# Optimization experiments

Hardware: AMD Instinct MI355X
Metric: run time of the kernel (lower is better)

Reference implementation:

```python
import jax, jax.numpy as jnp
import numpy as np

WS = 8       # window size
NH = 6       # num heads
SHIFT = 4    # ws//2 since index=1 (shifted)
EPS = 1e-6


def _rel_pos_index(ws):
    coords = np.stack(np.meshgrid(np.arange(ws), np.arange(ws), indexing='ij'))  # (2,ws,ws)
    cf = coords.reshape(2, -1)
    rel = (cf[:, :, None] - cf[:, None, :]).transpose(1, 2, 0)  # (N,N,2)
    rel[..., 0] += ws - 1
    rel[..., 1] += ws - 1
    rel[..., 0] *= 2 * ws - 1
    return rel.sum(-1)  # (N,N) int


def _attn_mask(H, W, ws, shift):
    img = np.zeros((H, W))
    slices = (slice(0, -ws), slice(-ws, -shift), slice(-shift, None))
    cnt = 0
    for h in slices:
        for w in slices:
            img[h, w] = cnt
            cnt += 1
    mw = img.reshape(H // ws, ws, W // ws, ws).transpose(0, 2, 1, 3).reshape(-1, ws * ws)
    am = mw[:, None, :] - mw[:, :, None]  # (nW,N,N): unsqueeze(1) - unsqueeze(2)
    return np.where(am != 0, -100.0, 0.0).astype(np.float32)


def layernorm2d(x, w, b):
    mu = x.mean(1, keepdims=True)
    var = ((x - mu) ** 2).mean(1, keepdims=True)
    y = (x - mu) / jnp.sqrt(var + EPS)
    return w[None, :, None, None] * y + b[None, :, None, None]


def window_partition(x, ws):
    B, C, H, W = x.shape
    x = x.reshape(B, C, H // ws, ws, W // ws, ws)
    return x.transpose(0, 2, 4, 3, 5, 1).reshape(-1, ws * ws, C)


def window_reverse(win, ws, H, W):
    B = win.shape[0] // ((H // ws) * (W // ws))
    x = win.reshape(B, H // ws, W // ws, ws, ws, -1)
    return x.transpose(0, 5, 1, 3, 2, 4).reshape(B, -1, H, W)


def shifted_window_attn(x, qkv_w, qkv_b, proj_w, proj_b, rpb_table):
    B, C, H, W = x.shape
    N = WS * WS
    hd = C // NH
    scale = hd ** -0.5
    # faithful to original: raw reshape BCHW->BHWC (reinterpretation), roll, reshape back
    x = jnp.roll(x.reshape(B, H, W, C), (-SHIFT, -SHIFT), (1, 2)).reshape(B, C, H, W)
    win = window_partition(x, WS)  # (B_, N, C)
    B_ = win.shape[0]
    qkv = (win @ qkv_w + qkv_b).reshape(B_, N, 3, NH, hd).transpose(2, 0, 3, 1, 4)
    q, k, v = qkv[0] * scale, qkv[1], qkv[2]
    attn = jnp.einsum('bhnd,bhmd->bhnm', q, k)  # (B_,NH,N,N)
    rpi = _rel_pos_index(WS)
    bias = rpb_table[rpi.reshape(-1)].reshape(N, N, NH).transpose(2, 0, 1)
    attn = attn + bias[None]
    mask = jnp.asarray(_attn_mask(H, W, WS, SHIFT))  # (nW,N,N)
    nW = mask.shape[0]
    attn = attn.reshape(B_ // nW, nW, NH, N, N) + mask[None, :, None]
    attn = jax.nn.softmax(attn.reshape(B_, NH, N, N), axis=-1)
    out = jnp.einsum('bhnm,bhmd->bhnd', attn, v).transpose(0, 2, 1, 3).reshape(B_, N, C)
    out = out @ proj_w + proj_b
    return window_reverse(out, WS, H, W)


def channel_attention(y, ca_w, ca_b):
    gap = y.mean((2, 3))  # (B,C)
    s = jnp.einsum('bc,oc->bo', gap, ca_w) + ca_b  # 1x1 conv on pooled feature
    return s[:, :, None, None]


def mlp(y, fc1_w, fc1_b, fc2_w, fc2_b):
    B, C, H, W = y.shape
    t = y.transpose(0, 2, 3, 1)  # (B,H,W,C)
    t = jax.nn.gelu(t @ fc1_w + fc1_b, approximate=False)
    t = t @ fc2_w + fc2_b
    return t.transpose(0, 3, 1, 2)


def setup_inputs() -> dict:
    key = jax.random.key(0)
    ks = jax.random.split(key, 8)
    C, H, W, B = 192, 256, 256, 2
    hid = 2 * C
    sc = 0.02
    return {
        'x': jax.random.normal(ks[0], (B, C, H, W), jnp.float32),
        'norm1_w': jnp.ones((C,), jnp.float32),
        'norm1_b': jnp.zeros((C,), jnp.float32),
        'qkv_w': jax.random.normal(ks[1], (C, 3 * C), jnp.float32) * sc,
        'qkv_b': jnp.zeros((3 * C,), jnp.float32),
        'proj_w': jax.random.normal(ks[2], (C, C), jnp.float32) * sc,
        'proj_b': jnp.zeros((C,), jnp.float32),
        'rpb_table': jax.random.normal(ks[3], ((2 * WS - 1) ** 2, NH), jnp.float32) * sc,
        'ca_w': jax.random.normal(ks[4], (C, C), jnp.float32) * sc,
        'ca_b': jnp.zeros((C,), jnp.float32),
        'norm2_w': jnp.ones((C,), jnp.float32),
        'norm2_b': jnp.zeros((C,), jnp.float32),
        'fc1_w': jax.random.normal(ks[5], (C, hid), jnp.float32) * sc,
        'fc1_b': jnp.zeros((hid,), jnp.float32),
        'fc2_w': jax.random.normal(ks[6], (hid, C), jnp.float32) * sc,
        'fc2_b': jnp.zeros((C,), jnp.float32),
    }


def reference(x, norm1_w, norm1_b, qkv_w, qkv_b, proj_w, proj_b, rpb_table,
              ca_w, ca_b, norm2_w, norm2_b, fc1_w, fc1_b, fc2_w, fc2_b):
    y = layernorm2d(x, norm1_w, norm1_b)
    y = shifted_window_attn(y, qkv_w, qkv_b, proj_w, proj_b, rpb_table)
    y = y * channel_attention(y, ca_w, ca_b)
    x = x + y
    y2 = mlp(layernorm2d(x, norm2_w, norm2_b), fc1_w, fc1_b, fc2_w, fc2_b)
    return x + y2
```

## Files before the change

kernel.cpp:

```cpp
#include <hip/hip_runtime.h>
#include <hip/hip_bf16.h>
#include <stdint.h>

#define C_   192
#define H_   256
#define W_   256
#define HW_  65536
#define CHW  12582912
#define NH_  6
#define HID_ 384

typedef __attribute__((ext_vector_type(8))) __bf16 bf16x8;
typedef __attribute__((ext_vector_type(4))) float  fx4;

__device__ __forceinline__ uint16_t f2bf(float f) {
  uint32_t u = __builtin_bit_cast(uint32_t, f);
  u += 0x7fffu + ((u >> 16) & 1u);
  return (uint16_t)(u >> 16);
}
__device__ __forceinline__ float bf2f(uint16_t h) {
  uint32_t u = ((uint32_t)h) << 16;
  return __builtin_bit_cast(float, u);
}
__device__ __forceinline__ uint32_t pk2(float a, float b) {
  return (uint32_t)f2bf(a) | ((uint32_t)f2bf(b) << 16);
}
__device__ __forceinline__ bf16x8 ld8(const uint16_t* p) {
  uint4 v = *reinterpret_cast<const uint4*>(p);
  return __builtin_bit_cast(bf16x8, v);
}
__device__ __forceinline__ fx4 mfma16(bf16x8 a, bf16x8 b, fx4 c) {
  return __builtin_amdgcn_mfma_f32_16x16x32_bf16(a, b, c, 0, 0, 0);
}

__global__ __launch_bounds__(256) void prep_kernel(
    const float* __restrict__ qkv_w, const float* __restrict__ proj_w,
    const float* __restrict__ fc1_w, const float* __restrict__ fc2_w,
    const float* __restrict__ rpb,
    uint16_t* __restrict__ qkv_wt, uint16_t* __restrict__ proj_wt,
    uint16_t* __restrict__ fc1_wt, uint16_t* __restrict__ fc2_wt,
    float* __restrict__ rpbb) {
  int tid = blockIdx.x * 256 + threadIdx.x;
  if (tid < 576 * 192) {
    int f = tid / 192, k = tid % 192;
    qkv_wt[tid] = f2bf(qkv_w[k * 576 + f]);
  }
  int t1 = tid - 576 * 192;
  if (t1 >= 0 && t1 < 192 * 192) {
    int f = t1 / 192, k = t1 % 192;
    proj_wt[t1] = f2bf(proj_w[k * 192 + f]);
  }
  int t2 = t1 - 192 * 192;
  if (t2 >= 0 && t2 < 384 * 192) {
    int f = t2 / 192, k = t2 % 192;
    fc1_wt[t2] = f2bf(fc1_w[k * 384 + f]);
  }
  int t3 = t2 - 384 * 192;
  if (t3 >= 0 && t3 < 192 * 384) {
    int f = t3 / 384, k = t3 % 384;
    fc2_wt[t3] = f2bf(fc2_w[k * 192 + f]);
  }
  int t4 = t3 - 192 * 384;
  if (t4 >= 0 && t4 < 6 * 64 * 64) {
    int h = t4 / 4096, nm = t4 % 4096, n = nm / 64, m = nm % 64;
    int yn = n >> 3, xn = n & 7, ym = m >> 3, xm = m & 7;
    int idx = (yn - ym + 7) * 15 + (xn - xm + 7);
    rpbb[t4] = rpb[idx * NH_ + h];
  }
}

__global__ __launch_bounds__(256) void ln1_stats(const float* __restrict__ x,
                                                 float* __restrict__ mu,
                                                 float* __restrict__ rsig) {
  int t = blockIdx.x * 256 + threadIdx.x;
  int b = t >> 16, hw = t & 65535;
  const float* xp = x + (size_t)b * CHW + hw;
  float s = 0.f, sq = 0.f;
#pragma unroll 8
  for (int c = 0; c < C_; c++) {
    float v = xp[(size_t)c * HW_];
    s += v; sq += v * v;
  }
  float m = s * (1.0f / C_);
  float var = sq * (1.0f / C_) - m * m;
  mu[t] = m;
  rsig[t] = rsqrtf(var + 1e-6f);
}

__global__ __launch_bounds__(256) void ln1_apply_kernel(
    const float* __restrict__ x, const float* __restrict__ mu, const float* __restrict__ rsig,
    const float* __restrict__ n1w, const float* __restrict__ n1b,
    uint16_t* __restrict__ y_tok) {
  __shared__ __attribute__((aligned(16))) uint16_t tile[192 * 66];
  int wg = blockIdx.x;
  int b = wg >> 10, hw0 = (wg & 1023) << 6;
  int t = threadIdx.x;
  const float* xb = x + (size_t)b * CHW;
  const float* mub = mu + b * HW_;
  const float* rsb = rsig + b * HW_;
#pragma unroll 4
  for (int it = 0; it < 48; it++) {
    int id = it * 256 + t;
    int ca = id >> 6, pp = id & 63;
    int g = ca * 65536 + hw0 + pp;
    int h2 = g / 49152;
    int r = g - h2 * 49152;
    int w2 = r / 192;
    int c2 = r - w2 * 192;
    int f = ((h2 + 4) & 255) * 49152 + ((w2 + 4) & 255) * 192 + c2;
    int cnat = f >> 16;
    int hwn = f & 65535;
    float v = (xb[f] - mub[hwn]) * rsb[hwn] * n1w[cnat] + n1b[cnat];
    tile[ca * 66 + pp] = f2bf(v);
  }
  __syncthreads();
  uint16_t* yb = y_tok + ((size_t)(b * HW_ + hw0)) * C_;
#pragma unroll 4
  for (int it = 0; it < 48; it++) {
    int id = it * 256 + t;
    int pp = id / 192, ca = id - pp * 192;
    yb[id] = tile[ca * 66 + pp];
  }
}

__global__ __launch_bounds__(256, 2) void attn_kernel(
    const uint16_t* __restrict__ y_tok, const uint16_t* __restrict__ qkv_wt,
    const float* __restrict__ qkv_b, const uint16_t* __restrict__ proj_wt,
    const float* __restrict__ proj_b, const float* __restrict__ rpbb,
    uint16_t* __restrict__ y_attn, float* __restrict__ part) {
  __shared__ __attribute__((aligned(16))) uint16_t Qs[64 * 200];
  __shared__ __attribute__((aligned(16))) uint16_t Ks[64 * 200];
  __shared__ __attribute__((aligned(16))) uint16_t VT[32 * 72];
  __shared__ __attribute__((aligned(16))) uint16_t Ps[64 * 72];
  const int wg = blockIdx.x;
  const int b = wg >> 10, wid = wg & 1023;
  const int wh = wid >> 5, ww = wid & 31;
  const int t = threadIdx.x;
  const int w = t >> 6, l = t & 63;
  const int lane16 = l & 15, quad = l >> 4;
  const int trow = w * 16 + quad * 4;

  bf16x8 afr[4][6];
#pragma unroll
  for (int m = 0; m < 4; m++) {
    const int tok = m * 16 + lane16;
    const uint16_t* ap = y_tok +
        ((size_t)(b * HW_ + (wh * 8 + (tok >> 3)) * W_ + ww * 8 + (tok & 7))) * C_ + quad * 8;
#pragma unroll
    for (int k = 0; k < 6; k++) afr[m][k] = ld8(ap + k * 32);
  }

  const float scale = 0.17677669529663687f;
  uint32_t vpack[3][4][2];

#pragma unroll
  for (int j = 0; j < 3; j++) {
    const int nt = w + 4 * j;
    const uint16_t* bp = qkv_wt + (nt * 16 + lane16) * C_ + quad * 8;
    bf16x8 bfr[6];
#pragma unroll
    for (int k = 0; k < 6; k++) bfr[k] = ld8(bp + k * 32);
    fx4 acc[4];
#pragma unroll
    for (int m = 0; m < 4; m++) acc[m] = fx4{0.f, 0.f, 0.f, 0.f};
#pragma unroll
    for (int k = 0; k < 6; k++)
#pragma unroll
      for (int m = 0; m < 4; m++) acc[m] = mfma16(afr[m][k], bfr[k], acc[m]);
    const int f = nt * 16 + lane16;
    const float bias = qkv_b[f];
#pragma unroll
    for (int m = 0; m < 4; m++)
#pragma unroll
      for (int r = 0; r < 4; r++)
        Qs[(m * 16 + quad * 4 + r) * 200 + f] = f2bf((acc[m][r] + bias) * scale);
  }
#pragma unroll
  for (int j = 3; j < 6; j++) {
    const int nt = w + 4 * j;
    const uint16_t* bp = qkv_wt + (nt * 16 + lane16) * C_ + quad * 8;
    bf16x8 bfr[6];
#pragma unroll
    for (int k = 0; k < 6; k++) bfr[k] = ld8(bp + k * 32);
    fx4 acc[4];
#pragma unroll
    for (int m = 0; m < 4; m++) acc[m] = fx4{0.f, 0.f, 0.f, 0.f};
#pragma unroll
    for (int k = 0; k < 6; k++)
#pragma unroll
      for (int m = 0; m < 4; m++) acc[m] = mfma16(afr[m][k], bfr[k], acc[m]);
    const int f = nt * 16 + lane16;
    const float bias = qkv_b[f];
#pragma unroll
    for (int m = 0; m < 4; m++)
#pragma unroll
      for (int r = 0; r < 4; r++)
        Ks[(m * 16 + quad * 4 + r) * 200 + (f - 192)] = f2bf(acc[m][r] + bias);
  }
#pragma unroll
  for (int j = 6; j < 9; j++) {
    const int nt = w + 4 * j;
    const uint16_t* bp = qkv_wt + (nt * 16 + lane16) * C_ + quad * 8;
    bf16x8 bfr[6];
#pragma unroll
    for (int k = 0; k < 6; k++) bfr[k] = ld8(bp + k * 32);
    fx4 acc[4];
#pragma unroll
    for (int m = 0; m < 4; m++) acc[m] = fx4{0.f, 0.f, 0.f, 0.f};
#pragma unroll
    for (int k = 0; k < 6; k++)
#pragma unroll
      for (int m = 0; m < 4; m++) acc[m] = mfma16(afr[m][k], bfr[k], acc[m]);
    const float bias = qkv_b[nt * 16 + lane16];
    const int jv = j - 6;
#pragma unroll
    for (int m = 0; m < 4; m++) {
      vpack[jv][m][0] = pk2(acc[m][0] + bias, acc[m][1] + bias);
      vpack[jv][m][1] = pk2(acc[m][2] + bias, acc[m][3] + bias);
    }
  }

  const bool whe = (wh == 31), wwe = (ww == 31);

  for (int h = 0; h < 6; h++) {
    __syncthreads();
    {
      const int vt0 = 2 * h, vt1 = 2 * h + 1;
      if (w == (vt0 & 3)) {
        const int jv = vt0 >> 2;
#pragma unroll
        for (int m = 0; m < 4; m++) {
          uint2 vv; vv.x = vpack[jv][m][0]; vv.y = vpack[jv][m][1];
          *reinterpret_cast<uint2*>(&VT[lane16 * 72 + m * 16 + quad * 4]) = vv;
        }
      }
      if (w == (vt1 & 3)) {
        const int jv = vt1 >> 2;
#pragma unroll
        for (int m = 0; m < 4; m++) {
          uint2 vv; vv.x = vpack[jv][m][0]; vv.y = vpack[jv][m][1];
          *reinterpret_cast<uint2*>(&VT[(16 + lane16) * 72 + m * 16 + quad * 4]) = vv;
        }
      }
    }
    __syncthreads();

    const bf16x8 qa = ld8(&Qs[(w * 16 + lane16) * 200 + h * 32 + quad * 8]);
    fx4 sacc[4];
#pragma unroll
    for (int nt = 0; nt < 4; nt++) {
      const bf16x8 kb = ld8(&Ks[(nt * 16 + lane16) * 200 + h * 32 + quad * 8]);
      fx4 z = {0.f, 0.f, 0.f, 0.f};
      sacc[nt] = mfma16(qa, kb, z);
    }
    const float* rb = rpbb + h * 4096;
#pragma unroll
    for (int nt = 0; nt < 4; nt++) {
      const int ct = nt * 16 + lane16;
      const bool rbc = whe && ((ct >> 3) >= 4);
      const bool cbc = wwe && ((ct & 7) >= 4);
#pragma unroll
      for (int r = 0; r < 4; r++) {
        const int rt = trow + r;
        const bool rbr = whe && ((rt >> 3) >= 4);
        const bool cbr = wwe && ((rt & 7) >= 4);
        float v = sacc[nt][r] + rb[rt * 64 + ct];
        if (rbr != rbc || cbr != cbc) v -= 100.f;
        sacc[nt][r] = v;
      }
    }
    float sm[4];
#pragma unroll
    for (int r = 0; r < 4; r++) {
      float m = fmaxf(fmaxf(sacc[0][r], sacc[1][r]), fmaxf(sacc[2][r], sacc[3][r]));
      m = fmaxf(m, __shfl_xor(m, 1));
      m = fmaxf(m, __shfl_xor(m, 2));
      m = fmaxf(m, __shfl_xor(m, 4));
      m = fmaxf(m, __shfl_xor(m, 8));
      float s0 = 0.f;
#pragma unroll
      for (int nt = 0; nt < 4; nt++) {
        float e = exp2f((sacc[nt][r] - m) * 1.4426950408889634f);
        sacc[nt][r] = e; s0 += e;
      }
      s0 += __shfl_xor(s0, 1);
      s0 += __shfl_xor(s0, 2);
      s0 += __shfl_xor(s0, 4);
      s0 += __shfl_xor(s0, 8);
      sm[r] = s0;
    }
#pragma unroll
    for (int nt = 0; nt < 4; nt++)
#pragma unroll
      for (int r = 0; r < 4; r++)
        Ps[(trow + r) * 72 + nt * 16 + lane16] = f2bf(sacc[nt][r]);
    fx4 o0 = {0.f, 0.f, 0.f, 0.f}, o1 = {0.f, 0.f, 0.f, 0.f};
#pragma unroll
    for (int ks2 = 0; ks2 < 2; ks2++) {
      const bf16x8 pa = ld8(&Ps[(w * 16 + lane16) * 72 + ks2 * 32 + quad * 8]);
      const bf16x8 v0 = ld8(&VT[(lane16) * 72 + ks2 * 32 + quad * 8]);
      const bf16x8 v1 = ld8(&VT[(16 + lane16) * 72 + ks2 * 32 + quad * 8]);
      o0 = mfma16(pa, v0, o0);
      o1 = mfma16(pa, v1, o1);
    }
#pragma unroll
    for (int r = 0; r < 4; r++) {
      const float inv = 1.0f / sm[r];
      Qs[(trow + r) * 200 + h * 32 + lane16] = f2bf(o0[r] * inv);
      Qs[(trow + r) * 200 + h * 32 + 16 + lane16] = f2bf(o1[r] * inv);
    }
  }
  __syncthreads();

  bf16x8 ofr[4][6];
#pragma unroll
  for (int m = 0; m < 4; m++)
#pragma unroll
    for (int k = 0; k < 6; k++)
      ofr[m][k] = ld8(&Qs[(m * 16 + lane16) * 200 + k * 32 + quad * 8]);

  uint16_t* yb = y_attn + (size_t)b * HW_ * C_;
  uint32_t obase[4][4];
#pragma unroll
  for (int m = 0; m < 4; m++)
#pragma unroll
    for (int r = 0; r < 4; r++) {
      const int tok = m * 16 + quad * 4 + r;
      obase[m][r] = (uint32_t)(((wh * 8 + (tok >> 3)) * W_ + ww * 8 + (tok & 7)) * C_);
    }
#pragma unroll
  for (int j = 0; j < 3; j++) {
    const int nt = w + 4 * j;
    const uint16_t* bp = proj_wt + (nt * 16 + lane16) * C_ + quad * 8;
    bf16x8 bfr[6];
#pragma unroll
    for (int k = 0; k < 6; k++) bfr[k] = ld8(bp + k * 32);
    fx4 acc[4];
#pragma unroll
    for (int m = 0; m < 4; m++) acc[m] = fx4{0.f, 0.f, 0.f, 0.f};
#pragma unroll
    for (int k = 0; k < 6; k++)
#pragma unroll
      for (int m = 0; m < 4; m++) acc[m] = mfma16(ofr[m][k], bfr[k], acc[m]);
    const float pb = proj_b[nt * 16 + lane16];
    float cs = 0.f;
#pragma unroll
    for (int m = 0; m < 4; m++)
#pragma unroll
      for (int r = 0; r < 4; r++) {
        const float v = acc[m][r] + pb;
        yb[obase[m][r] + nt * 16 + lane16] = f2bf(v);
        cs += v;
      }
    cs += __shfl_xor(cs, 16);
    cs += __shfl_xor(cs, 32);
    if (l < 16) part[(size_t)wg * 192 + nt * 16 + lane16] = cs;
  }
}

__global__ __launch_bounds__(768) void ca_s_kernel(const float* __restrict__ part,
                                                   const float* __restrict__ ca_w,
                                                   const float* __restrict__ ca_b,
                                                   float* __restrict__ sbuf) {
  int b = blockIdx.x;
  int t = threadIdx.x;
  __shared__ float red[768];
  __shared__ float gap[192];
  int g = t / 192, c = t - g * 192;
  float s = 0.f;
#pragma unroll 8
  for (int i = g; i < 1024; i += 4) s += part[((size_t)b * 1024 + i) * 192 + c];
  red[t] = s;
  __syncthreads();
  if (t < 192)
    gap[t] = (red[t] + red[t + 192] + red[t + 384] + red[t + 576]) * (1.0f / 65536.0f);
  __syncthreads();
  if (t < 192) {
    float acc = ca_b[t];
#pragma unroll 8
    for (int c2 = 0; c2 < 192; c2++) acc += gap[c2] * ca_w[t * 192 + c2];
    sbuf[b * 192 + t] = acc;
  }
}

__global__ __launch_bounds__(256, 3) void resid_ln2(
    const float* __restrict__ x, const uint16_t* __restrict__ y_attn,
    const float* __restrict__ sbuf, const float* __restrict__ n2w,
    const float* __restrict__ n2b, uint16_t* __restrict__ t2) {
  __shared__ __attribute__((aligned(16))) float tile[192 * 66];
  __shared__ float red[512];
  __shared__ float mus[128];
  int wg = blockIdx.x;
  int b = wg >> 10, hw0 = (wg & 1023) << 6;
  int t = threadIdx.x;
#pragma unroll 4
  for (int it = 0; it < 48; it++) {
    int id = it * 256 + t;
    int c = id >> 6, p = id & 63;
    tile[c * 66 + p] = x[(size_t)b * CHW + (size_t)c * HW_ + hw0 + p];
  }
  __syncthreads();
#pragma unroll 4
  for (int it = 0; it < 48; it++) {
    int id = it * 256 + t;
    int p = id / 192, c = id - p * 192;
    float y = bf2f(y_attn[((size_t)(b * HW_ + hw0 + p)) * C_ + c]);
    tile[c * 66 + p] += sbuf[b * 192 + c] * y;
  }
  __syncthreads();
  {
    int p = t & 63, g = t >> 6;
    float s = 0.f, sq = 0.f;
    for (int c = g * 48; c < g * 48 + 48; c++) {
      float v = tile[c * 66 + p];
      s += v; sq += v * v;
    }
    red[g * 64 + p] = s;
    red[256 + g * 64 + p] = sq;
  }
  __syncthreads();
  if (t < 64) {
    float ss = red[t] + red[64 + t] + red[128 + t] + red[192 + t];
    float qq = red[256 + t] + red[320 + t] + red[384 + t] + red[448 + t];
    float m = ss * (1.0f / C_);
    float var = qq * (1.0f / C_) - m * m;
    mus[t] = m;
    mus[64 + t] = rsqrtf(var + 1e-6f);
  }
  __syncthreads();
#pragma unroll 4
  for (int it = 0; it < 48; it++) {
    int id = it * 256 + t;
    int p = id / 192, c = id - p * 192;
    float v = (tile[c * 66 + p] - mus[p]) * mus[64 + p] * n2w[c] + n2b[c];
    t2[((size_t)(b * HW_ + hw0 + p)) * C_ + c] = f2bf(v);
  }
}

__global__ __launch_bounds__(256, 3) void mlp_kernel(
    const uint16_t* __restrict__ t2, const uint16_t* __restrict__ fc1_wt,
    const float* __restrict__ fc1_b, const uint16_t* __restrict__ fc2_wt,
    const float* __restrict__ fc2_b, const float* __restrict__ x,
    const uint16_t* __restrict__ y_attn, const float* __restrict__ sbuf,
    float* __restrict__ out) {
  __shared__ __attribute__((aligned(16))) char smem[192 * 66 * 4];
  __shared__ float sarr[192];
  uint16_t* hbuf = (uint16_t*)smem;
  float* ftile = (float*)smem;
  int wg = blockIdx.x;
  int b = wg >> 10, hw0 = (wg & 1023) << 6;
  int t = threadIdx.x;
  int w = t >> 6, l = t & 63;
  int lane16 = l & 15, quad = l >> 4;
  if (t < 192) sarr[t] = sbuf[b * 192 + t];

  bf16x8 afr[4][6];
  const uint16_t* ab = t2 + ((size_t)(b * HW_ + hw0)) * C_;
#pragma unroll
  for (int m = 0; m < 4; m++) {
    const uint16_t* ap = ab + (m * 16 + lane16) * C_ + quad * 8;
#pragma unroll
    for (int k = 0; k < 6; k++) afr[m][k] = ld8(ap + k * 32);
  }

#pragma unroll
  for (int j = 0; j < 6; j++) {
    const int nt = w + 4 * j;
    const uint16_t* bp = fc1_wt + (nt * 16 + lane16) * C_ + quad * 8;
    bf16x8 bfr[6];
#pragma unroll
    for (int k = 0; k < 6; k++) bfr[k] = ld8(bp + k * 32);
    fx4 acc[4];
#pragma unroll
    for (int m = 0; m < 4; m++) acc[m] = fx4{0.f, 0.f, 0.f, 0.f};
#pragma unroll
    for (int k = 0; k < 6; k++)
#pragma unroll
      for (int m = 0; m < 4; m++) acc[m] = mfma16(afr[m][k], bfr[k], acc[m]);
    const float bias = fc1_b[nt * 16 + lane16];
#pragma unroll
    for (int m = 0; m < 4; m++)
#pragma unroll
      for (int r = 0; r < 4; r++) {
        float v = acc[m][r] + bias;
        float ge = 0.5f * v * (1.0f + erff(v * 0.7071067811865476f));
        hbuf[(m * 16 + quad * 4 + r) * 392 + nt * 16 + lane16] = f2bf(ge);
      }
  }
  __syncthreads();

  fx4 acc2[3][4];
#pragma unroll
  for (int j = 0; j < 3; j++)
#pragma unroll
    for (int m = 0; m < 4; m++) acc2[j][m] = fx4{0.f, 0.f, 0.f, 0.f};
#pragma unroll
  for (int kc = 0; kc < 4; kc++) {
    bf16x8 ha[4][3];
#pragma unroll
    for (int m = 0; m < 4; m++)
#pragma unroll
      for (int kk = 0; kk < 3; kk++)
        ha[m][kk] = ld8(&hbuf[(m * 16 + lane16) * 392 + kc * 96 + kk * 32 + quad * 8]);
#pragma unroll
    for (int j = 0; j < 3; j++) {
      const int nt = w + 4 * j;
      const uint16_t* bp = fc2_wt + (nt * 16 + lane16) * HID_ + kc * 96 + quad * 8;
#pragma unroll
      for (int kk = 0; kk < 3; kk++) {
        const bf16x8 bb = ld8(bp + kk * 32);
#pragma unroll
        for (int m = 0; m < 4; m++) acc2[j][m] = mfma16(ha[m][kk], bb, acc2[j][m]);
      }
    }
  }
  __syncthreads();

#pragma unroll
  for (int j = 0; j < 3; j++) {
    const int nt = w + 4 * j;
    const float bias = fc2_b[nt * 16 + lane16];
#pragma unroll
    for (int m = 0; m < 4; m++) {
      float* fp = &ftile[(nt * 16 + lane16) * 66 + m * 16 + quad * 4];
      float2 a = {acc2[j][m][0] + bias, acc2[j][m][1] + bias};
      float2 b2 = {acc2[j][m][2] + bias, acc2[j][m][3] + bias};
      *reinterpret_cast<float2*>(fp) = a;
      *reinterpret_cast<float2*>(fp + 2) = b2;
    }
  }
  __syncthreads();
#pragma unroll 4
  for (int it = 0; it < 48; it++) {
    int id = it * 256 + t;
    int p = id / 192, c = id - p * 192;
    float y = bf2f(y_attn[((size_t)(b * HW_ + hw0 + p)) * C_ + c]);
    ftile[c * 66 + p] += sarr[c] * y;
  }
  __syncthreads();
#pragma unroll 4
  for (int it = 0; it < 48; it++) {
    int id = it * 256 + t;
    int c = id >> 6, p = id & 63;
    size_t gi = (size_t)b * CHW + (size_t)c * HW_ + hw0 + p;
    out[gi] = x[gi] + ftile[c * 66 + p];
  }
}

extern "C" void kernel_launch(void* const* d_in, const int* in_sizes, int n_in,
                              void* d_out, int out_size, void* d_ws, size_t ws_size,
                              hipStream_t stream) {
  const float* x      = (const float*)d_in[0];
  const float* n1w    = (const float*)d_in[1];
  const float* n1b    = (const float*)d_in[2];
  const float* qkv_w  = (const float*)d_in[3];
  const float* qkv_b  = (const float*)d_in[4];
  const float* proj_w = (const float*)d_in[5];
  const float* proj_b = (const float*)d_in[6];
  const float* rpb    = (const float*)d_in[7];
  const float* ca_w   = (const float*)d_in[8];
  const float* ca_b   = (const float*)d_in[9];
  const float* n2w    = (const float*)d_in[10];
  const float* n2b    = (const float*)d_in[11];
  const float* fc1_w  = (const float*)d_in[12];
  const float* fc1_b  = (const float*)d_in[13];
  const float* fc2_w  = (const float*)d_in[14];
  const float* fc2_b  = (const float*)d_in[15];
  float* out = (float*)d_out;

  char* ws = (char*)d_ws;
  uint16_t* y_tok   = (uint16_t*)(ws + 0);
  uint16_t* y_attn  = (uint16_t*)(ws + 50331648);
  uint16_t* t2      = y_tok;
  float*    mu      = (float*)   (ws + 100663296);
  float*    rsig    = (float*)   (ws + 101187584);
  uint16_t* qkv_wt  = (uint16_t*)(ws + 101711872);
  uint16_t* proj_wt = (uint16_t*)(ws + 101933056);
  uint16_t* fc1_wt  = (uint16_t*)(ws + 102006784);
  uint16_t* fc2_wt  = (uint16_t*)(ws + 102154240);
  float*    rpbb    = (float*)   (ws + 102301696);
  float*    part    = (float*)   (ws + 102400000);
  float*    sbuf    = (float*)   (ws + 103972864);

  hipLaunchKernelGGL(prep_kernel, dim3(1248), dim3(256), 0, stream,
                     qkv_w, proj_w, fc1_w, fc2_w, rpb, qkv_wt, proj_wt, fc1_wt, fc2_wt, rpbb);
  hipLaunchKernelGGL(ln1_stats, dim3(512), dim3(256), 0, stream, x, mu, rsig);
  hipLaunchKernelGGL(ln1_apply_kernel, dim3(2048), dim3(256), 0, stream,
                     x, mu, rsig, n1w, n1b, y_tok);
  hipLaunchKernelGGL(attn_kernel, dim3(2048), dim3(256), 0, stream,
                     y_tok, qkv_wt, qkv_b, proj_wt, proj_b, rpbb, y_attn, part);
  hipLaunchKernelGGL(ca_s_kernel, dim3(2), dim3(768), 0, stream, part, ca_w, ca_b, sbuf);
  hipLaunchKernelGGL(resid_ln2, dim3(2048), dim3(256), 0, stream,
                     x, y_attn, sbuf, n2w, n2b, t2);
  hipLaunchKernelGGL(mlp_kernel, dim3(2048), dim3(256), 0, stream,
                     t2, fc1_wt, fc1_b, fc2_wt, fc2_b, x, y_attn, sbuf, out);
}
```

Baseline: 577.5 us.

## Fuse residual+LayerNorm2 into MLP kernel and fold norm affine into fc1

Merges resid_ln2 and mlp_kernel into one 512-thread kernel. LayerNorm is applied in registers straight from the shared tile into MFMA A-fragments, so the bf16 t2 intermediate is never written to or read back from global memory. The norm2 weight and bias are folded into fc1 weights and a precomputed bias in prep, and erf-GELU is replaced by a tanh approximation built on exp2/rcp. Global loads are vectorized. The cost is changed numerics from the tanh GELU and the folded bf16 weights, plus higher register and LDS pressure at 512 threads.

```diff
diff --git a/kernel.cpp b/kernel.cpp
--- a/kernel.cpp
+++ b/kernel.cpp
@@ -11,6 +11,7 @@
 #define HID_ 384
 
 typedef __attribute__((ext_vector_type(8))) __bf16 bf16x8;
+typedef __attribute__((ext_vector_type(8))) uint16_t u16x8;
 typedef __attribute__((ext_vector_type(4))) float  fx4;
 
 __device__ __forceinline__ uint16_t f2bf(float f) {
@@ -32,14 +33,23 @@
 __device__ __forceinline__ fx4 mfma16(bf16x8 a, bf16x8 b, fx4 c) {
   return __builtin_amdgcn_mfma_f32_16x16x32_bf16(a, b, c, 0, 0, 0);
 }
+__device__ __forceinline__ float gelu_f(float v) {
+  float c2 = v * v;
+  float u = __builtin_fmaf(c2, 0.044715f, 1.0f) * v;
+  float e = exp2f(u * 2.3022084f);
+  float th = 1.0f - 2.0f * __builtin_amdgcn_rcpf(1.0f + e);
+  float hv = 0.5f * v;
+  return __builtin_fmaf(hv, th, hv);
+}
 
 __global__ __launch_bounds__(256) void prep_kernel(
     const float* __restrict__ qkv_w, const float* __restrict__ proj_w,
     const float* __restrict__ fc1_w, const float* __restrict__ fc2_w,
-    const float* __restrict__ rpb,
+    const float* __restrict__ rpb, const float* __restrict__ n2w,
+    const float* __restrict__ n2b, const float* __restrict__ fc1_b,
     uint16_t* __restrict__ qkv_wt, uint16_t* __restrict__ proj_wt,
     uint16_t* __restrict__ fc1_wt, uint16_t* __restrict__ fc2_wt,
-    float* __restrict__ rpbb) {
+    float* __restrict__ rpbb, float* __restrict__ b1f) {
   int tid = blockIdx.x * 256 + threadIdx.x;
   if (tid < 576 * 192) {
     int f = tid / 192, k = tid % 192;
@@ -53,7 +63,7 @@
   int t2 = t1 - 192 * 192;
   if (t2 >= 0 && t2 < 384 * 192) {
     int f = t2 / 192, k = t2 % 192;
-    fc1_wt[t2] = f2bf(fc1_w[k * 384 + f]);
+    fc1_wt[t2] = f2bf(fc1_w[k * 384 + f] * n2w[k]);
   }
   int t3 = t2 - 384 * 192;
   if (t3 >= 0 && t3 < 192 * 384) {
@@ -66,6 +76,12 @@
     int yn = n >> 3, xn = n & 7, ym = m >> 3, xm = m & 7;
     int idx = (yn - ym + 7) * 15 + (xn - xm + 7);
     rpbb[t4] = rpb[idx * NH_ + h];
+  }
+  int t5 = t4 - 6 * 64 * 64;
+  if (t5 >= 0 && t5 < 384) {
+    float acc = fc1_b[t5];
+    for (int c = 0; c < 192; c++) acc = __builtin_fmaf(n2b[c], fc1_w[c * 384 + t5], acc);
+    b1f[t5] = acc;
   }
 }
 
@@ -383,36 +399,59 @@
   }
 }
 
-__global__ __launch_bounds__(256, 3) void resid_ln2(
+__global__ __launch_bounds__(512, 6) void fused_mlp(
     const float* __restrict__ x, const uint16_t* __restrict__ y_attn,
-    const float* __restrict__ sbuf, const float* __restrict__ n2w,
-    const float* __restrict__ n2b, uint16_t* __restrict__ t2) {
-  __shared__ __attribute__((aligned(16))) float tile[192 * 66];
+    const float* __restrict__ sbuf,
+    const uint16_t* __restrict__ fc1_wt, const float* __restrict__ b1f,
+    const uint16_t* __restrict__ fc2_wt, const float* __restrict__ fc2_b,
+    float* __restrict__ out) {
+  __shared__ __attribute__((aligned(16))) char smem[192 * 66 * 4];
   __shared__ float red[512];
   __shared__ float mus[128];
-  int wg = blockIdx.x;
-  int b = wg >> 10, hw0 = (wg & 1023) << 6;
-  int t = threadIdx.x;
-#pragma unroll 4
-  for (int it = 0; it < 48; it++) {
-    int id = it * 256 + t;
-    int c = id >> 6, p = id & 63;
-    tile[c * 66 + p] = x[(size_t)b * CHW + (size_t)c * HW_ + hw0 + p];
-  }
-  __syncthreads();
-#pragma unroll 4
-  for (int it = 0; it < 48; it++) {
-    int id = it * 256 + t;
-    int p = id / 192, c = id - p * 192;
-    float y = bf2f(y_attn[((size_t)(b * HW_ + hw0 + p)) * C_ + c]);
-    tile[c * 66 + p] += sbuf[b * 192 + c] * y;
-  }
-  __syncthreads();
+  __shared__ float sarr[192];
+  float* tileXR = (float*)smem;
+  uint16_t* hbuf = (uint16_t*)smem;
+  float* ftile = (float*)smem;
+  const int wg = blockIdx.x;
+  const int b = wg >> 10, hw0 = (wg & 1023) << 6;
+  const int t = threadIdx.x;
+  const int w = t >> 6, l = t & 63;
+  const int lane16 = l & 15, quad = l >> 4;
+
+  if (t < 192) sarr[t] = sbuf[b * 192 + t];
+
+  const float* xb = x + (size_t)b * CHW + hw0;
+#pragma unroll
+  for (int i = 0; i < 12; i++) {
+    int id = i * 512 + t;
+    int c = id >> 5, p2 = id & 31;
+    float2 v = *reinterpret_cast<const float2*>(xb + (size_t)c * HW_ + p2 * 2);
+    *reinterpret_cast<float2*>(&tileXR[c * 66 + p2 * 2]) = v;
+  }
+  __syncthreads();
+
   {
+    const int p = t & 63, qb = (t >> 6) * 3;
+    const uint16_t* yr = y_attn + ((size_t)(b * HW_ + hw0 + p)) * C_;
+#pragma unroll
+    for (int i = 0; i < 3; i++) {
+      int q = qb + i;
+      u16x8 uv = __builtin_bit_cast(u16x8, ld8(yr + q * 8));
+#pragma unroll
+      for (int j = 0; j < 8; j++) {
+        int c = q * 8 + j;
+        tileXR[c * 66 + p] += sarr[c] * bf2f(uv[j]);
+      }
+    }
+  }
+  __syncthreads();
+
+  if (t < 256) {
     int p = t & 63, g = t >> 6;
     float s = 0.f, sq = 0.f;
+#pragma unroll 8
     for (int c = g * 48; c < g * 48 + 48; c++) {
-      float v = tile[c * 66 + p];
+      float v = tileXR[c * 66 + p];
       s += v; sq += v * v;
     }
     red[g * 64 + p] = s;
@@ -428,89 +467,81 @@
     mus[64 + t] = rsqrtf(var + 1e-6f);
   }
   __syncthreads();
+
+  bf16x8 afr[6];
+  const int m1 = w & 3;
+  {
+    const int p = m1 * 16 + lane16;
+    const float mu = mus[p], rs = mus[64 + p];
+#pragma unroll
+    for (int k = 0; k < 6; k++) {
+      uint32_t u0, u1, u2, u3;
+      {
+        int c = k * 32 + quad * 8;
+        float a0 = (tileXR[(c + 0) * 66 + p] - mu) * rs;
+        float a1 = (tileXR[(c + 1) * 66 + p] - mu) * rs;
+        float a2 = (tileXR[(c + 2) * 66 + p] - mu) * rs;
+        float a3 = (tileXR[(c + 3) * 66 + p] - mu) * rs;
+        float a4 = (tileXR[(c + 4) * 66 + p] - mu) * rs;
+        float a5 = (tileXR[(c + 5) * 66 + p] - mu) * rs;
+        float a6 = (tileXR[(c + 6) * 66 + p] - mu) * rs;
+        float a7 = (tileXR[(c + 7) * 66 + p] - mu) * rs;
+        u0 = pk2(a0, a1); u1 = pk2(a2, a3); u2 = pk2(a4, a5); u3 = pk2(a6, a7);
+      }
+      uint4 uv = {u0, u1, u2, u3};
+      afr[k] = __builtin_bit_cast(bf16x8, uv);
+    }
+  }
+  __syncthreads();
+
+  {
+    const int ntb = (w >> 2) * 12;
 #pragma unroll 4
-  for (int it = 0; it < 48; it++) {
-    int id = it * 256 + t;
-    int p = id / 192, c = id - p * 192;
-    float v = (tile[c * 66 + p] - mus[p]) * mus[64 + p] * n2w[c] + n2b[c];
-    t2[((size_t)(b * HW_ + hw0 + p)) * C_ + c] = f2bf(v);
-  }
-}
-
-__global__ __launch_bounds__(256, 3) void mlp_kernel(
-    const uint16_t* __restrict__ t2, const uint16_t* __restrict__ fc1_wt,
-    const float* __restrict__ fc1_b, const uint16_t* __restrict__ fc2_wt,
-    const float* __restrict__ fc2_b, const float* __restrict__ x,
-    const uint16_t* __restrict__ y_attn, const float* __restrict__ sbuf,
-    float* __restrict__ out) {
-  __shared__ __attribute__((aligned(16))) char smem[192 * 66 * 4];
-  __shared__ float sarr[192];
-  uint16_t* hbuf = (uint16_t*)smem;
-  float* ftile = (float*)smem;
-  int wg = blockIdx.x;
-  int b = wg >> 10, hw0 = (wg & 1023) << 6;
-  int t = threadIdx.x;
-  int w = t >> 6, l = t & 63;
-  int lane16 = l & 15, quad = l >> 4;
-  if (t < 192) sarr[t] = sbuf[b * 192 + t];
-
-  bf16x8 afr[4][6];
-  const uint16_t* ab = t2 + ((size_t)(b * HW_ + hw0)) * C_;
-#pragma unroll
-  for (int m = 0; m < 4; m++) {
-    const uint16_t* ap = ab + (m * 16 + lane16) * C_ + quad * 8;
-#pragma unroll
-    for (int k = 0; k < 6; k++) afr[m][k] = ld8(ap + k * 32);
-  }
-
-#pragma unroll
-  for (int j = 0; j < 6; j++) {
-    const int nt = w + 4 * j;
-    const uint16_t* bp = fc1_wt + (nt * 16 + lane16) * C_ + quad * 8;
-    bf16x8 bfr[6];
-#pragma unroll
-    for (int k = 0; k < 6; k++) bfr[k] = ld8(bp + k * 32);
-    fx4 acc[4];
-#pragma unroll
-    for (int m = 0; m < 4; m++) acc[m] = fx4{0.f, 0.f, 0.f, 0.f};
-#pragma unroll
-    for (int k = 0; k < 6; k++)
-#pragma unroll
-      for (int m = 0; m < 4; m++) acc[m] = mfma16(afr[m][k], bfr[k], acc[m]);
-    const float bias = fc1_b[nt * 16 + lane16];
-#pragma unroll
-    for (int m = 0; m < 4; m++)
-#pragma unroll
-      for (int r = 0; r < 4; r++) {
-        float v = acc[m][r] + bias;
-        float ge = 0.5f * v * (1.0f + erff(v * 0.7071067811865476f));
-        hbuf[(m * 16 + quad * 4 + r) * 392 + nt * 16 + lane16] = f2bf(ge);
-      }
-  }
-  __syncthreads();
-
-  fx4 acc2[3][4];
+    for (int j = 0; j < 12; j++) {
+      const int nt = ntb + j;
+      const uint16_t* bp = fc1_wt + (nt * 16 + lane16) * C_ + quad * 8;
+      bf16x8 bfr[6];
+#pragma unroll
+      for (int k = 0; k < 6; k++) bfr[k] = ld8(bp + k * 32);
+      fx4 acc = {0.f, 0.f, 0.f, 0.f};
+#pragma unroll
+      for (int k = 0; k < 6; k++) acc = mfma16(bfr[k], afr[k], acc);
+      const fx4 b4 = *reinterpret_cast<const fx4*>(b1f + nt * 16 + quad * 4);
+      float g0 = gelu_f(acc[0] + b4[0]);
+      float g1 = gelu_f(acc[1] + b4[1]);
+      float g2 = gelu_f(acc[2] + b4[2]);
+      float g3 = gelu_f(acc[3] + b4[3]);
+      uint2 wv = {pk2(g0, g1), pk2(g2, g3)};
+      *reinterpret_cast<uint2*>(&hbuf[(m1 * 16 + lane16) * 392 + nt * 16 + quad * 4]) = wv;
+    }
+  }
+  __syncthreads();
+
+  const int mh2 = w >> 2;
+  const int ntr2 = w & 3;
+  fx4 acc2[3][2];
 #pragma unroll
   for (int j = 0; j < 3; j++)
 #pragma unroll
-    for (int m = 0; m < 4; m++) acc2[j][m] = fx4{0.f, 0.f, 0.f, 0.f};
+    for (int mi = 0; mi < 2; mi++) acc2[j][mi] = fx4{0.f, 0.f, 0.f, 0.f};
 #pragma unroll
   for (int kc = 0; kc < 4; kc++) {
-    bf16x8 ha[4][3];
-#pragma unroll
-    for (int m = 0; m < 4; m++)
+    bf16x8 ha[2][3];
+#pragma unroll
+    for (int mi = 0; mi < 2; mi++)
 #pragma unroll
       for (int kk = 0; kk < 3; kk++)
-        ha[m][kk] = ld8(&hbuf[(m * 16 + lane16) * 392 + kc * 96 + kk * 32 + quad * 8]);
+        ha[mi][kk] = ld8(&hbuf[((mh2 * 2 + mi) * 16 + lane16) * 392 + kc * 96 + kk * 32 + quad * 8]);
 #pragma unroll
     for (int j = 0; j < 3; j++) {
-      const int nt = w + 4 * j;
-      const uint16_t* bp = fc2_wt + (nt * 16 + lane16) * HID_ + kc * 96 + quad * 8;
+      const int nt2 = ntr2 * 3 + j;
+      const uint16_t* bp = fc2_wt + (nt2 * 16 + lane16) * HID_ + kc * 96 + quad * 8;
 #pragma unroll
       for (int kk = 0; kk < 3; kk++) {
         const bf16x8 bb = ld8(bp + kk * 32);
 #pragma unroll
-        for (int m = 0; m < 4; m++) acc2[j][m] = mfma16(ha[m][kk], bb, acc2[j][m]);
+        for (int mi = 0; mi < 2; mi++)
+          acc2[j][mi] = mfma16(ha[mi][kk], bb, acc2[j][mi]);
       }
     }
   }
@@ -518,32 +549,44 @@
 
 #pragma unroll
   for (int j = 0; j < 3; j++) {
-    const int nt = w + 4 * j;
-    const float bias = fc2_b[nt * 16 + lane16];
-#pragma unroll
-    for (int m = 0; m < 4; m++) {
-      float* fp = &ftile[(nt * 16 + lane16) * 66 + m * 16 + quad * 4];
-      float2 a = {acc2[j][m][0] + bias, acc2[j][m][1] + bias};
-      float2 b2 = {acc2[j][m][2] + bias, acc2[j][m][3] + bias};
-      *reinterpret_cast<float2*>(fp) = a;
-      *reinterpret_cast<float2*>(fp + 2) = b2;
-    }
-  }
-  __syncthreads();
-#pragma unroll 4
-  for (int it = 0; it < 48; it++) {
-    int id = it * 256 + t;
-    int p = id / 192, c = id - p * 192;
-    float y = bf2f(y_attn[((size_t)(b * HW_ + hw0 + p)) * C_ + c]);
-    ftile[c * 66 + p] += sarr[c] * y;
-  }
-  __syncthreads();
-#pragma unroll 4
-  for (int it = 0; it < 48; it++) {
-    int id = it * 256 + t;
-    int c = id >> 6, p = id & 63;
-    size_t gi = (size_t)b * CHW + (size_t)c * HW_ + hw0 + p;
-    out[gi] = x[gi] + ftile[c * 66 + p];
+    const int nt2 = ntr2 * 3 + j;
+    const float bias = fc2_b[nt2 * 16 + lane16];
+#pragma unroll
+    for (int mi = 0; mi < 2; mi++) {
+      float* fp = &ftile[(nt2 * 16 + lane16) * 66 + (mh2 * 2 + mi) * 16 + quad * 4];
+      float2 aa = {acc2[j][mi][0] + bias, acc2[j][mi][1] + bias};
+      float2 bb2 = {acc2[j][mi][2] + bias, acc2[j][mi][3] + bias};
+      *reinterpret_cast<float2*>(fp) = aa;
+      *reinterpret_cast<float2*>(fp + 2) = bb2;
+    }
+  }
+  __syncthreads();
+
+  {
+    const int p = t & 63, qb = (t >> 6) * 3;
+    const uint16_t* yr = y_attn + ((size_t)(b * HW_ + hw0 + p)) * C_;
+#pragma unroll
+    for (int i = 0; i < 3; i++) {
+      int q = qb + i;
+      u16x8 uv = __builtin_bit_cast(u16x8, ld8(yr + q * 8));
+#pragma unroll
+      for (int j = 0; j < 8; j++) {
+        int c = q * 8 + j;
+        ftile[c * 66 + p] += sarr[c] * bf2f(uv[j]);
+      }
+    }
+  }
+  __syncthreads();
+
+  float* ob = out + (size_t)b * CHW + hw0;
+#pragma unroll
+  for (int i = 0; i < 12; i++) {
+    int id = i * 512 + t;
+    int c = id >> 5, p2 = id & 31;
+    float2 xv = *reinterpret_cast<const float2*>(xb + (size_t)c * HW_ + p2 * 2);
+    float2 fv = *reinterpret_cast<const float2*>(&ftile[c * 66 + p2 * 2]);
+    float2 ov = {xv.x + fv.x, xv.y + fv.y};
+    *reinterpret_cast<float2*>(ob + (size_t)c * HW_ + p2 * 2) = ov;
   }
 }
 
@@ -571,7 +614,6 @@
   char* ws = (char*)d_ws;
   uint16_t* y_tok   = (uint16_t*)(ws + 0);
   uint16_t* y_attn  = (uint16_t*)(ws + 50331648);
-  uint16_t* t2      = y_tok;
   float*    mu      = (float*)   (ws + 100663296);
   float*    rsig    = (float*)   (ws + 101187584);
   uint16_t* qkv_wt  = (uint16_t*)(ws + 101711872);
@@ -581,17 +623,17 @@
   float*    rpbb    = (float*)   (ws + 102301696);
   float*    part    = (float*)   (ws + 102400000);
   float*    sbuf    = (float*)   (ws + 103972864);
-
-  hipLaunchKernelGGL(prep_kernel, dim3(1248), dim3(256), 0, stream,
-                     qkv_w, proj_w, fc1_w, fc2_w, rpb, qkv_wt, proj_wt, fc1_wt, fc2_wt, rpbb);
+  float*    b1f     = (float*)   (ws + 103974400);
+
+  hipLaunchKernelGGL(prep_kernel, dim3(1250), dim3(256), 0, stream,
+                     qkv_w, proj_w, fc1_w, fc2_w, rpb, n2w, n2b, fc1_b,
+                     qkv_wt, proj_wt, fc1_wt, fc2_wt, rpbb, b1f);
   hipLaunchKernelGGL(ln1_stats, dim3(512), dim3(256), 0, stream, x, mu, rsig);
   hipLaunchKernelGGL(ln1_apply_kernel, dim3(2048), dim3(256), 0, stream,
                      x, mu, rsig, n1w, n1b, y_tok);
   hipLaunchKernelGGL(attn_kernel, dim3(2048), dim3(256), 0, stream,
                      y_tok, qkv_wt, qkv_b, proj_wt, proj_b, rpbb, y_attn, part);
   hipLaunchKernelGGL(ca_s_kernel, dim3(2), dim3(768), 0, stream, part, ca_w, ca_b, sbuf);
-  hipLaunchKernelGGL(resid_ln2, dim3(2048), dim3(256), 0, stream,
-                     x, y_attn, sbuf, n2w, n2b, t2);
-  hipLaunchKernelGGL(mlp_kernel, dim3(2048), dim3(256), 0, stream,
-                     t2, fc1_wt, fc1_b, fc2_wt, fc2_b, x, y_attn, sbuf, out);
-}
+  hipLaunchKernelGGL(fused_mlp, dim3(2048), dim3(512), 0, stream,
+                     x, y_attn, sbuf, fc1_wt, b1f, fc2_wt, fc2_b, out);
+}
```

Result: slower. 687.6 us (+19.1%).

## Use tanh-approx GELU, transpose fc1 MFMA output, and split channel-attention reduction

Applied to the files above, without the earlier changes.

Replaces erf-based GELU in the MLP with a tanh-form approximation built on exp2 and a fast reciprocal. The fc1 MFMA operands are swapped so each lane holds four consecutive columns, which allows a vector bias load and packed 8-byte stores into the LDS hidden buffer. The channel-attention global average pool, previously done by only 2 blocks, is split into a 128-block partial reduction plus a small second kernel. These target the erf cost, scattered LDS writes and a serial low-occupancy reduction, at the cost of an extra launch and GELU approximation error.

```diff
diff --git a/kernel.cpp b/kernel.cpp
--- a/kernel.cpp
+++ b/kernel.cpp
@@ -11,6 +11,7 @@
 #define HID_ 384
 
 typedef __attribute__((ext_vector_type(8))) __bf16 bf16x8;
+typedef __attribute__((ext_vector_type(8))) uint16_t u16x8;
 typedef __attribute__((ext_vector_type(4))) float  fx4;
 
 __device__ __forceinline__ uint16_t f2bf(float f) {
@@ -31,6 +32,14 @@
 }
 __device__ __forceinline__ fx4 mfma16(bf16x8 a, bf16x8 b, fx4 c) {
   return __builtin_amdgcn_mfma_f32_16x16x32_bf16(a, b, c, 0, 0, 0);
+}
+__device__ __forceinline__ float gelu_f(float v) {
+  float c2 = v * v;
+  float u = __builtin_fmaf(c2, 0.044715f, 1.0f) * v;
+  float e = exp2f(u * 2.3022084f);
+  float th = 1.0f - 2.0f * __builtin_amdgcn_rcpf(1.0f + e);
+  float hv = 0.5f * v;
+  return __builtin_fmaf(hv, th, hv);
 }
 
 __global__ __launch_bounds__(256) void prep_kernel(
@@ -358,29 +367,34 @@
   }
 }
 
-__global__ __launch_bounds__(768) void ca_s_kernel(const float* __restrict__ part,
-                                                   const float* __restrict__ ca_w,
-                                                   const float* __restrict__ ca_b,
-                                                   float* __restrict__ sbuf) {
+__global__ __launch_bounds__(192) void ca_gap(const float* __restrict__ part,
+                                              float* __restrict__ gpart) {
+  int blk = blockIdx.x;
+  int b = blk >> 6, ch = blk & 63;
+  int c = threadIdx.x;
+  float s = 0.f;
+#pragma unroll
+  for (int i = 0; i < 16; i++)
+    s += part[((size_t)b * 1024 + ch * 16 + i) * 192 + c];
+  gpart[blk * 192 + c] = s;
+}
+
+__global__ __launch_bounds__(192) void ca_s2(const float* __restrict__ gpart,
+                                             const float* __restrict__ ca_w,
+                                             const float* __restrict__ ca_b,
+                                             float* __restrict__ sbuf) {
   int b = blockIdx.x;
   int t = threadIdx.x;
-  __shared__ float red[768];
   __shared__ float gap[192];
-  int g = t / 192, c = t - g * 192;
   float s = 0.f;
 #pragma unroll 8
-  for (int i = g; i < 1024; i += 4) s += part[((size_t)b * 1024 + i) * 192 + c];
-  red[t] = s;
-  __syncthreads();
-  if (t < 192)
-    gap[t] = (red[t] + red[t + 192] + red[t + 384] + red[t + 576]) * (1.0f / 65536.0f);
-  __syncthreads();
-  if (t < 192) {
-    float acc = ca_b[t];
+  for (int i = 0; i < 64; i++) s += gpart[(b * 64 + i) * 192 + t];
+  gap[t] = s * (1.0f / 65536.0f);
+  __syncthreads();
+  float acc = ca_b[t];
 #pragma unroll 8
-    for (int c2 = 0; c2 < 192; c2++) acc += gap[c2] * ca_w[t * 192 + c2];
-    sbuf[b * 192 + t] = acc;
-  }
+  for (int c2 = 0; c2 < 192; c2++) acc += gap[c2] * ca_w[t * 192 + c2];
+  sbuf[b * 192 + t] = acc;
 }
 
 __global__ __launch_bounds__(256, 3) void resid_ln2(
@@ -476,16 +490,17 @@
 #pragma unroll
     for (int k = 0; k < 6; k++)
 #pragma unroll
-      for (int m = 0; m < 4; m++) acc[m] = mfma16(afr[m][k], bfr[k], acc[m]);
-    const float bias = fc1_b[nt * 16 + lane16];
-#pragma unroll
-    for (int m = 0; m < 4; m++)
-#pragma unroll
-      for (int r = 0; r < 4; r++) {
-        float v = acc[m][r] + bias;
-        float ge = 0.5f * v * (1.0f + erff(v * 0.7071067811865476f));
-        hbuf[(m * 16 + quad * 4 + r) * 392 + nt * 16 + lane16] = f2bf(ge);
-      }
+      for (int m = 0; m < 4; m++) acc[m] = mfma16(bfr[k], afr[m][k], acc[m]);
+    const fx4 bv = *reinterpret_cast<const fx4*>(fc1_b + nt * 16 + quad * 4);
+#pragma unroll
+    for (int m = 0; m < 4; m++) {
+      float g0 = gelu_f(acc[m][0] + bv[0]);
+      float g1 = gelu_f(acc[m][1] + bv[1]);
+      float g2 = gelu_f(acc[m][2] + bv[2]);
+      float g3 = gelu_f(acc[m][3] + bv[3]);
+      uint2 wv = {pk2(g0, g1), pk2(g2, g3)};
+      *reinterpret_cast<uint2*>(&hbuf[(m * 16 + lane16) * 392 + nt * 16 + quad * 4]) = wv;
+    }
   }
   __syncthreads();
 
@@ -581,6 +596,7 @@
   float*    rpbb    = (float*)   (ws + 102301696);
   float*    part    = (float*)   (ws + 102400000);
   float*    sbuf    = (float*)   (ws + 103972864);
+  float*    gpart   = (float*)   (ws + 103974400);
 
   hipLaunchKernelGGL(prep_kernel, dim3(1248), dim3(256), 0, stream,
                      qkv_w, proj_w, fc1_w, fc2_w, rpb, qkv_wt, proj_wt, fc1_wt, fc2_wt, rpbb);
@@ -589,7 +605,8 @@
                      x, mu, rsig, n1w, n1b, y_tok);
   hipLaunchKernelGGL(attn_kernel, dim3(2048), dim3(256), 0, stream,
                      y_tok, qkv_wt, qkv_b, proj_wt, proj_b, rpbb, y_attn, part);
-  hipLaunchKernelGGL(ca_s_kernel, dim3(2), dim3(768), 0, stream, part, ca_w, ca_b, sbuf);
+  hipLaunchKernelGGL(ca_gap, dim3(128), dim3(192), 0, stream, part, gpart);
+  hipLaunchKernelGGL(ca_s2, dim3(2), dim3(192), 0, stream, gpart, ca_w, ca_b, sbuf);
   hipLaunchKernelGGL(resid_ln2, dim3(2048), dim3(256), 0, stream,
                      x, y_attn, sbuf, n2w, n2b, t2);
   hipLaunchKernelGGL(mlp_kernel, dim3(2048), dim3(256), 0, stream,
```

Measured after the change: 526.2 us. 8.9% less time.
